# Kernel tuning notes

Hardware: AMD Instinct MI355X
Metric: run time of the kernel (lower is better)

The kernel has to match this reference:

```python
import jax, jax.numpy as jnp
import numpy as np

B, S, D_MODEL = 2, 2048, 4096
N_HEADS, N_KV, HEAD_DIM = 32, 8, 128
N_GROUPS = N_HEADS // N_KV
QKV_DIM = (N_HEADS + 2 * N_KV) * HEAD_DIM


def _rope_tables(seq_len, head_dim, base=10000.0):
    inv_freq = 1.0 / (base ** (np.arange(0, head_dim, 2, dtype=np.float32) / head_dim))
    t = np.arange(seq_len, dtype=np.float32)
    freqs = np.outer(t, inv_freq)                      # [S, D/2]
    emb = np.concatenate([freqs, freqs], axis=-1)      # [S, D]
    return jnp.asarray(np.cos(emb)), jnp.asarray(np.sin(emb))


def setup_inputs() -> dict:
    key = jax.random.key(0)
    k1, k2, k3 = jax.random.split(key, 3)
    cos, sin = _rope_tables(S, HEAD_DIM)
    return {
        "hidden_states": jax.random.normal(k1, (B, S, D_MODEL), dtype=jnp.float32),
        "cos": cos,
        "sin": sin,
        "W_qkv": jax.random.normal(k2, (D_MODEL, QKV_DIM), dtype=jnp.float32) * (D_MODEL ** -0.5),
        "W_out": jax.random.normal(k3, (D_MODEL, D_MODEL), dtype=jnp.float32) * (D_MODEL ** -0.5),
    }


def _rotate_half(x):
    x1, x2 = jnp.split(x, 2, axis=-1)
    return jnp.concatenate([-x2, x1], axis=-1)


def _apply_rope(x, cos, sin):
    # x: [b, h, s, d]; cos/sin: [s, d]
    c = cos[None, None, :, :]
    s = sin[None, None, :, :]
    return x * c + _rotate_half(x) * s


def reference(hidden_states, cos, sin, W_qkv, W_out):
    b, s, _ = hidden_states.shape
    qkv = jnp.einsum("bsm,mq->bsq", hidden_states, W_qkv)
    q_end = N_HEADS * HEAD_DIM
    kv_sz = N_KV * HEAD_DIM
    q = qkv[..., :q_end].reshape(b, s, N_HEADS, HEAD_DIM).transpose(0, 2, 1, 3)
    k = qkv[..., q_end:q_end + kv_sz].reshape(b, s, N_KV, HEAD_DIM).transpose(0, 2, 1, 3)
    v = qkv[..., q_end + kv_sz:].reshape(b, s, N_KV, HEAD_DIM).transpose(0, 2, 1, 3)

    q = _apply_rope(q, cos, sin)          # [b, H, s, d]
    k = _apply_rope(k, cos, sin)          # [b, KV, s, d] (equiv. to repeat->rope->stride slice)

    # GQA without materializing repeated KV: group query heads per KV head.
    qg = q.reshape(b, N_KV, N_GROUPS, s, HEAD_DIM)
    scale = HEAD_DIM ** -0.5
    scores = jnp.einsum("bkgqd,bkpd->bkgqp", qg, k) * scale  # [b, KV, G, s, s]
    causal = jnp.tril(jnp.ones((s, s), dtype=bool))
    scores = jnp.where(causal, scores, jnp.finfo(scores.dtype).min)
    probs = jax.nn.softmax(scores, axis=-1)
    out = jnp.einsum("bkgqp,bkpd->bkgqd", probs, v)           # [b, KV, G, s, d]
    out = out.reshape(b, N_HEADS, s, HEAD_DIM).transpose(0, 2, 1, 3).reshape(b, s, D_MODEL)
    return jnp.einsum("bsm,mn->bsn", out, W_out)
```

## Files before the change

kernel.cpp:

```cpp
#include <hip/hip_runtime.h>


typedef __bf16 bf16;
typedef bf16 bf16x8 __attribute__((ext_vector_type(8)));
typedef bf16 bf16x4 __attribute__((ext_vector_type(4)));
typedef float f32x4 __attribute__((ext_vector_type(4)));
typedef unsigned int u32;
typedef u32 u32x4 __attribute__((ext_vector_type(4)));

#define B_ 2
#define S_ 2048
#define DM 4096
#define NH 32
#define NKV 8
#define HD 128
#define QKV_DIM 6144

typedef __attribute__((address_space(3))) void lds_void;
typedef const __attribute__((address_space(1))) void glb_void;

__device__ __forceinline__ void gld_lds16(const bf16* g, bf16* l) {
  __builtin_amdgcn_global_load_lds((glb_void*)g, (lds_void*)l, 16, 0, 0);
}

__device__ __forceinline__ u32 bf16bits(float x) {
  union { bf16 h; unsigned short s; } u;
  u.h = (bf16)x;
  return (u32)u.s;
}

__global__ __launch_bounds__(256) void cast_f32_bf16(const float* __restrict__ src,
                                                     bf16* __restrict__ dst, int n) {
  int i = (blockIdx.x * 256 + threadIdx.x) * 4;
  float4 v = *(const float4*)(src + i);
  bf16x4 o;
  o[0] = (bf16)v.x; o[1] = (bf16)v.y; o[2] = (bf16)v.z; o[3] = (bf16)v.w;
  *(bf16x4*)(dst + i) = o;
}

__global__ __launch_bounds__(256) void transpose_cast_w(const float* __restrict__ W,
                                                        bf16* __restrict__ Wt,
                                                        int K, int N) {
  __shared__ float tile[64][65];
  const int n0 = blockIdx.x * 64, k0 = blockIdx.y * 64;
  const int t = threadIdx.x, j = t & 63, i0 = t >> 6;
  for (int p = 0; p < 16; ++p) {
    int i = i0 + p * 4;
    tile[i][j] = W[(size_t)(k0 + i) * N + n0 + j];
  }
  __syncthreads();
  for (int p = 0; p < 16; ++p) {
    int n = i0 + p * 4;
    Wt[(size_t)(n0 + n) * K + k0 + j] = (bf16)tile[j][n];
  }
}

__global__ __launch_bounds__(256) void transpose_v(const bf16* __restrict__ qkv,
                                                   bf16* __restrict__ v_t) {
  __shared__ bf16 tile[64][65];
  const int s0 = blockIdx.x * 64;
  const int d0 = blockIdx.y * 64;
  const int bk = blockIdx.z;
  const int b = bk >> 3, kv = bk & 7;
  const int t = threadIdx.x, j = t & 63, i0 = t >> 6;
  const bf16* src = qkv + (size_t)b * S_ * QKV_DIM + 5120 + kv * HD;
  for (int p = 0; p < 16; ++p) {
    int i = i0 + p * 4;
    tile[i][j] = src[(size_t)(s0 + i) * QKV_DIM + d0 + j];
  }
  __syncthreads();
  bf16* dst = v_t + ((size_t)bk * HD + d0) * S_ + s0;
  for (int p = 0; p < 16; ++p) {
    int dd = i0 + p * 4;
    dst[(size_t)dd * S_ + j] = tile[j][dd];
  }
}

__global__ __launch_bounds__(128) void rope_kernel(const bf16* __restrict__ qkv,
                                                   const float* __restrict__ cosT,
                                                   const float* __restrict__ sinT,
                                                   bf16* __restrict__ q_r,
                                                   bf16* __restrict__ k_r) {
  const int bs = blockIdx.x;
  const int b = bs >> 11, s = bs & 2047;
  const int d = threadIdx.x;
  const float cv = cosT[s * HD + d];
  const float sv = sinT[s * HD + d];
  const bf16* row = qkv + (size_t)bs * QKV_DIM;
  const float scale = 0.08838834764831845f;
  for (int h = 0; h < NH; ++h) {
    float x = (float)row[h * HD + d];
    float xr = (d < 64) ? -(float)row[h * HD + d + 64] : (float)row[h * HD + d - 64];
    q_r[(((size_t)(b * NH + h)) * S_ + s) * HD + d] = (bf16)((x * cv + xr * sv) * scale);
  }
  for (int kv = 0; kv < NKV; ++kv) {
    float x = (float)row[DM + kv * HD + d];
    float xr = (d < 64) ? -(float)row[DM + kv * HD + d + 64] : (float)row[DM + kv * HD + d - 64];
    k_r[(((size_t)(b * NKV + kv)) * S_ + s) * HD + d] = (bf16)(x * cv + xr * sv);
  }
}

template <bool OUT_BF16>
__global__ __launch_bounds__(256) void gemm_bt(const bf16* __restrict__ A,
                                               const bf16* __restrict__ Bt,
                                               void* __restrict__ Cout,
                                               int M, int N, int K) {
  __shared__ bf16 As[128 * 32];
  __shared__ bf16 Bs[128 * 32];
  const int m0 = blockIdx.y * 128, n0 = blockIdx.x * 128;
  const int t = threadIdx.x;
  const int lane = t & 63, w = t >> 6;
  const int wm = (w >> 1) * 64, wn = (w & 1) * 64;
  const int quad = lane >> 4, c = lane & 15;

  f32x4 acc[4][4] = {};

  const int s0i = t;
  const int r0 = s0i >> 2, c0 = (s0i & 3) * 8;
  const int s1i = 256 + t;
  const int r1 = s1i >> 2, c1 = (s1i & 3) * 8;
  const bf16* Ap0 = A + (size_t)(m0 + r0) * K + c0;
  const bf16* Ap1 = A + (size_t)(m0 + r1) * K + c1;
  const bf16* Bp0 = Bt + (size_t)(n0 + r0) * K + c0;
  const bf16* Bp1 = Bt + (size_t)(n0 + r1) * K + c1;
  bf16* Asl0 = As + (size_t)(w * 64) * 8;
  bf16* Asl1 = As + (size_t)(256 + w * 64) * 8;
  bf16* Bsl0 = Bs + (size_t)(w * 64) * 8;
  bf16* Bsl1 = Bs + (size_t)(256 + w * 64) * 8;

  for (int k0 = 0; k0 < K; k0 += 32) {
    gld_lds16(Ap0 + k0, Asl0);
    gld_lds16(Ap1 + k0, Asl1);
    gld_lds16(Bp0 + k0, Bsl0);
    gld_lds16(Bp1 + k0, Bsl1);
    __syncthreads();

    bf16x8 af[4], bfr[4];
#pragma unroll
    for (int i = 0; i < 4; ++i)
      af[i] = *(const bf16x8*)(As + (wm + i * 16 + c) * 32 + quad * 8);
#pragma unroll
    for (int j = 0; j < 4; ++j)
      bfr[j] = *(const bf16x8*)(Bs + (wn + j * 16 + c) * 32 + quad * 8);
#pragma unroll
    for (int i = 0; i < 4; ++i)
#pragma unroll
      for (int j = 0; j < 4; ++j)
        acc[i][j] = __builtin_amdgcn_mfma_f32_16x16x32_bf16(af[i], bfr[j], acc[i][j], 0, 0, 0);
    __syncthreads();
  }

#pragma unroll
  for (int i = 0; i < 4; ++i)
#pragma unroll
    for (int j = 0; j < 4; ++j) {
      const int row = m0 + wm + i * 16 + quad * 4;
      const int col = n0 + wn + j * 16 + c;
      if constexpr (OUT_BF16) {
        bf16* Cp = (bf16*)Cout;
#pragma unroll
        for (int r = 0; r < 4; ++r) Cp[(size_t)(row + r) * N + col] = (bf16)acc[i][j][r];
      } else {
        float* Cp = (float*)Cout;
#pragma unroll
        for (int r = 0; r < 4; ++r) Cp[(size_t)(row + r) * N + col] = acc[i][j][r];
      }
    }
}

#define SKS 136
#define SVS 40
__global__ __launch_bounds__(256) void attn_kernel(const bf16* __restrict__ q_r,
                                                   const bf16* __restrict__ k_r,
                                                   const bf16* __restrict__ v_t,
                                                   bf16* __restrict__ attn_out) {
  __shared__ bf16 Ks[32 * SKS];
  __shared__ bf16 Vs[128 * SVS];

  const int bh = blockIdx.x;
  const int b = bh >> 5, h = bh & 31;
  const int kv = h >> 2;
  const int q0 = blockIdx.y * 64;
  const int t = threadIdx.x, w = t >> 6, lane = t & 63;
  const int quad = lane >> 4, c = lane & 15;
  const int myq = q0 + w * 16 + c;

  const bf16* qrow = q_r + ((size_t)(b * NH + h) * S_ + myq) * HD;
  bf16x8 qf[4];
#pragma unroll
  for (int kk = 0; kk < 4; ++kk) qf[kk] = *(const bf16x8*)(qrow + quad * 8 + kk * 32);

  float m_i = -1e30f, l_i = 0.f;
  f32x4 o_acc[8];
#pragma unroll
  for (int n = 0; n < 8; ++n) o_acc[n] = (f32x4){0.f, 0.f, 0.f, 0.f};

  const bf16* kb_ptr = k_r + (size_t)(b * NKV + kv) * S_ * HD;
  const bf16* vb_ptr = v_t + (size_t)(b * NKV + kv) * HD * S_;

  const int nch = (q0 + 64) >> 5;
  const int ks_key = t >> 3, ks_doff = (t & 7) * 16;
  const int vs_d = t >> 1, vs_koff = (t & 1) * 16;
  const int src0 = c + 32 * (quad & 1);
  const int src1 = src0 + 16;
  const bool hiTile = (quad & 2) != 0;

  for (int ch = 0; ch < nch; ++ch) {
    const int kb = ch * 32;
    __syncthreads();
    {
      const bf16* kp = kb_ptr + (size_t)(kb + ks_key) * HD + ks_doff;
      bf16x8 kv0 = *(const bf16x8*)(kp);
      bf16x8 kv1 = *(const bf16x8*)(kp + 8);
      const bf16* vp = vb_ptr + (size_t)vs_d * S_ + kb + vs_koff;
      bf16x8 vv0 = *(const bf16x8*)(vp);
      bf16x8 vv1 = *(const bf16x8*)(vp + 8);
      *(bf16x8*)(Ks + ks_key * SKS + ks_doff) = kv0;
      *(bf16x8*)(Ks + ks_key * SKS + ks_doff + 8) = kv1;
      *(bf16x8*)(Vs + vs_d * SVS + vs_koff) = vv0;
      *(bf16x8*)(Vs + vs_d * SVS + vs_koff + 8) = vv1;
    }
    __syncthreads();

    if (kb <= q0 + w * 16 + 15) {
      f32x4 st0 = (f32x4){0.f, 0.f, 0.f, 0.f};
      f32x4 st1 = (f32x4){0.f, 0.f, 0.f, 0.f};
#pragma unroll
      for (int kk = 0; kk < 4; ++kk) {
        bf16x8 kf0 = *(const bf16x8*)(Ks + c * SKS + quad * 8 + kk * 32);
        bf16x8 kf1 = *(const bf16x8*)(Ks + (16 + c) * SKS + quad * 8 + kk * 32);
        st0 = __builtin_amdgcn_mfma_f32_16x16x32_bf16(kf0, qf[kk], st0, 0, 0, 0);
        st1 = __builtin_amdgcn_mfma_f32_16x16x32_bf16(kf1, qf[kk], st1, 0, 0, 0);
      }

      float v0[4], v1[4];
      const bool needMask = (kb + 31 > q0 + w * 16);
#pragma unroll
      for (int r = 0; r < 4; ++r) { v0[r] = st0[r]; v1[r] = st1[r]; }
      if (needMask) {
        const int key0 = kb + quad * 4;
#pragma unroll
        for (int r = 0; r < 4; ++r) {
          if (key0 + r > myq) v0[r] = -1e30f;
          if (key0 + 16 + r > myq) v1[r] = -1e30f;
        }
      }

      float mloc = fmaxf(fmaxf(fmaxf(v0[0], v0[1]), fmaxf(v0[2], v0[3])),
                         fmaxf(fmaxf(v1[0], v1[1]), fmaxf(v1[2], v1[3])));
      mloc = fmaxf(mloc, __shfl_xor(mloc, 16, 64));
      mloc = fmaxf(mloc, __shfl_xor(mloc, 32, 64));
      const float mnew = fmaxf(m_i, mloc);
      float e0[4], e1[4];
      float sum = 0.f;
#pragma unroll
      for (int r = 0; r < 4; ++r) {
        e0[r] = __expf(v0[r] - mnew);
        e1[r] = __expf(v1[r] - mnew);
        sum += e0[r] + e1[r];
      }
      sum += __shfl_xor(sum, 16, 64);
      sum += __shfl_xor(sum, 32, 64);
      const float alpha = __expf(m_i - mnew);
      m_i = mnew;
      l_i = l_i * alpha + sum;

      u32 pk[4];
#pragma unroll
      for (int r = 0; r < 4; ++r) pk[r] = bf16bits(e0[r]) | (bf16bits(e1[r]) << 16);
      u32 a0[4], a1[4];
#pragma unroll
      for (int r = 0; r < 4; ++r) {
        a0[r] = (u32)__shfl((int)pk[r], src0, 64);
        a1[r] = (u32)__shfl((int)pk[r], src1, 64);
      }
      u32 w0, w1, w2, w3;
      if (hiTile) {
        w0 = (a0[0] >> 16) | (a0[1] & 0xffff0000u);
        w1 = (a0[2] >> 16) | (a0[3] & 0xffff0000u);
        w2 = (a1[0] >> 16) | (a1[1] & 0xffff0000u);
        w3 = (a1[2] >> 16) | (a1[3] & 0xffff0000u);
      } else {
        w0 = (a0[0] & 0xffffu) | (a0[1] << 16);
        w1 = (a0[2] & 0xffffu) | (a0[3] << 16);
        w2 = (a1[0] & 0xffffu) | (a1[1] << 16);
        w3 = (a1[2] & 0xffffu) | (a1[3] << 16);
      }
      bf16x8 pf = __builtin_bit_cast(bf16x8, (u32x4){w0, w1, w2, w3});

      float alpha_o[4];
#pragma unroll
      for (int r = 0; r < 4; ++r) alpha_o[r] = __shfl(alpha, quad * 4 + r, 64);

#pragma unroll
      for (int n = 0; n < 8; ++n) {
#pragma unroll
        for (int r = 0; r < 4; ++r) o_acc[n][r] *= alpha_o[r];
      }
#pragma unroll
      for (int n = 0; n < 8; ++n) {
        bf16x8 vf = *(const bf16x8*)(Vs + (n * 16 + c) * SVS + quad * 8);
        o_acc[n] = __builtin_amdgcn_mfma_f32_16x16x32_bf16(pf, vf, o_acc[n], 0, 0, 0);
      }
    }
  }

  float l_o[4];
#pragma unroll
  for (int r = 0; r < 4; ++r) l_o[r] = __shfl(l_i, quad * 4 + r, 64);
#pragma unroll
  for (int n = 0; n < 8; ++n)
#pragma unroll
    for (int r = 0; r < 4; ++r) {
      const int row = q0 + w * 16 + quad * 4 + r;
      const float ov = o_acc[n][r] / l_o[r];
      attn_out[((size_t)b * S_ + row) * DM + h * HD + n * 16 + c] = (bf16)ov;
    }
}

extern "C" void kernel_launch(void* const* d_in, const int* in_sizes, int n_in,
                              void* d_out, int out_size, void* d_ws, size_t ws_size,
                              hipStream_t stream) {
  const float* hidden = (const float*)d_in[0];
  const float* cosT = (const float*)d_in[1];
  const float* sinT = (const float*)d_in[2];
  const float* Wqkv = (const float*)d_in[3];
  const float* Wout = (const float*)d_in[4];
  float* out = (float*)d_out;
  char* ws = (char*)d_ws;

  bf16* WqkvT = (bf16*)(ws + 0);
  bf16* q_r = (bf16*)(ws + 0);
  bf16* k_r = (bf16*)(ws + 33554432);
  bf16* WoutT = (bf16*)(ws + 50331648);
  bf16* h_bf = (bf16*)(ws + 83886080);
  bf16* attn_out = (bf16*)(ws + 83886080);
  bf16* v_t = (bf16*)(ws + 117440512);
  bf16* qkv = (bf16*)d_out;

  cast_f32_bf16<<<dim3(16384), dim3(256), 0, stream>>>(hidden, h_bf, B_ * S_ * DM);
  transpose_cast_w<<<dim3(QKV_DIM / 64, DM / 64), dim3(256), 0, stream>>>(Wqkv, WqkvT, DM, QKV_DIM);
  transpose_cast_w<<<dim3(DM / 64, DM / 64), dim3(256), 0, stream>>>(Wout, WoutT, DM, DM);
  gemm_bt<true><<<dim3(QKV_DIM / 128, (B_ * S_) / 128), dim3(256), 0, stream>>>(
      h_bf, WqkvT, (void*)qkv, B_ * S_, QKV_DIM, DM);
  rope_kernel<<<dim3(B_ * S_), dim3(128), 0, stream>>>(qkv, cosT, sinT, q_r, k_r);
  transpose_v<<<dim3(S_ / 64, HD / 64, B_ * NKV), dim3(256), 0, stream>>>(qkv, v_t);
  attn_kernel<<<dim3(B_ * NH, S_ / 64), dim3(256), 0, stream>>>(q_r, k_r, v_t, attn_out);
  gemm_bt<false><<<dim3(DM / 128, (B_ * S_) / 128), dim3(256), 0, stream>>>(
      attn_out, WoutT, (void*)out, B_ * S_, DM, DM);
}
```

Baseline: 933.1 us.

## Rewrite GEMMs with large double-buffered swizzled tiles and widen attention KV blocks

Replaces the 128x128 GEMM with a 512-thread templated kernel using large tiles (128x384 for QKV, 256x256 for output). It double-buffers 64-wide K slices in dynamic LDS with XOR swizzling, raw barriers, vmcnt waits, setprio around the MFMA blocks and a grid remap for locality. The attention kernel moves to 64-key chunks, prefetches the next K/V chunk into registers, and skips the rescale of running max and output when the max grows by no more than 8. These changes target memory stalls, LDS bank conflicts and per-iteration overhead, at the cost of much higher register and LDS pressure.

```diff
diff --git a/kernel.cpp b/kernel.cpp
--- a/kernel.cpp
+++ b/kernel.cpp
@@ -28,6 +28,12 @@
   u.h = (bf16)x;
   return (u32)u.s;
 }
+
+#define BAR() __builtin_amdgcn_s_barrier()
+#define VM4() asm volatile("s_waitcnt vmcnt(4)" ::: "memory")
+#define VM0() asm volatile("s_waitcnt vmcnt(0)" ::: "memory")
+#define PRIO1() __builtin_amdgcn_s_setprio(1)
+#define PRIO0() __builtin_amdgcn_s_setprio(0)
 
 __global__ __launch_bounds__(256) void cast_f32_bf16(const float* __restrict__ src,
                                                      bf16* __restrict__ dst, int n) {
@@ -100,81 +106,137 @@
   }
 }
 
-template <bool OUT_BF16>
-__global__ __launch_bounds__(256) void gemm_bt(const bf16* __restrict__ A,
-                                               const bf16* __restrict__ Bt,
-                                               void* __restrict__ Cout,
-                                               int M, int N, int K) {
-  __shared__ bf16 As[128 * 32];
-  __shared__ bf16 Bs[128 * 32];
-  const int m0 = blockIdx.y * 128, n0 = blockIdx.x * 128;
+template <bool OUT_BF16, int BM, int BN>
+__global__ __launch_bounds__(512, 2) void gemm_bt(const bf16* __restrict__ A,
+                                                  const bf16* __restrict__ Bt,
+                                                  void* __restrict__ Cout,
+                                                  int M, int N, int K) {
+  constexpr int MF = BM / 32;
+  constexpr int NF = BN / 64;
+  constexpr int NCA = BM / 128;
+  constexpr int NCB = BN / 128;
+  constexpr int AKH = BM * 64;
+  constexpr int BKH = BN * 64;
+  constexpr int BUF = 2 * (AKH + BKH);
+  extern __shared__ char lds[];
+  const int NT = K >> 6;
+
+  const int nwg = gridDim.x;
+  const int cpx = nwg >> 3;
+  const int wg = (blockIdx.x & 7) * cpx + (blockIdx.x >> 3);
+  const int nbx = N / BN;
+  const int bx = wg % nbx, by = wg / nbx;
+  const int m0 = by * BM, n0 = bx * BN;
+
   const int t = threadIdx.x;
-  const int lane = t & 63, w = t >> 6;
-  const int wm = (w >> 1) * 64, wn = (w & 1) * 64;
+  const int w = t >> 6, lane = t & 63;
+  const int wr = w >> 2, wc = w & 3;
   const int quad = lane >> 4, c = lane & 15;
 
-  f32x4 acc[4][4] = {};
-
-  const int s0i = t;
-  const int r0 = s0i >> 2, c0 = (s0i & 3) * 8;
-  const int s1i = 256 + t;
-  const int r1 = s1i >> 2, c1 = (s1i & 3) * 8;
-  const bf16* Ap0 = A + (size_t)(m0 + r0) * K + c0;
-  const bf16* Ap1 = A + (size_t)(m0 + r1) * K + c1;
-  const bf16* Bp0 = Bt + (size_t)(n0 + r0) * K + c0;
-  const bf16* Bp1 = Bt + (size_t)(n0 + r1) * K + c1;
-  bf16* Asl0 = As + (size_t)(w * 64) * 8;
-  bf16* Asl1 = As + (size_t)(256 + w * 64) * 8;
-  bf16* Bsl0 = Bs + (size_t)(w * 64) * 8;
-  bf16* Bsl1 = Bs + (size_t)(256 + w * 64) * 8;
-
-  for (int k0 = 0; k0 < K; k0 += 32) {
-    gld_lds16(Ap0 + k0, Asl0);
-    gld_lds16(Ap1 + k0, Asl1);
-    gld_lds16(Bp0 + k0, Bsl0);
-    gld_lds16(Bp1 + k0, Bsl1);
-    __syncthreads();
-
-    bf16x8 af[4], bfr[4];
-#pragma unroll
-    for (int i = 0; i < 4; ++i)
-      af[i] = *(const bf16x8*)(As + (wm + i * 16 + c) * 32 + quad * 8);
-#pragma unroll
-    for (int j = 0; j < 4; ++j)
-      bfr[j] = *(const bf16x8*)(Bs + (wn + j * 16 + c) * 32 + quad * 8);
-#pragma unroll
-    for (int i = 0; i < 4; ++i)
-#pragma unroll
-      for (int j = 0; j < 4; ++j)
-        acc[i][j] = __builtin_amdgcn_mfma_f32_16x16x32_bf16(af[i], bfr[j], acc[i][j], 0, 0, 0);
-    __syncthreads();
-  }
-
-#pragma unroll
-  for (int i = 0; i < 4; ++i)
-#pragma unroll
-    for (int j = 0; j < 4; ++j) {
-      const int row = m0 + wm + i * 16 + quad * 4;
-      const int col = n0 + wn + j * 16 + c;
+  const int aOff = (((wr * (BM / 2) + c) * 64 + quad * 16) ^ ((c & 8) << 2));
+  const int bOff = 2 * AKH + ((((wc * (BN / 4) + c) * 64 + quad * 16) ^ ((c & 8) << 2)));
+
+  const int scol = (((lane & 3) ^ ((lane >> 4) & 2)) << 3);
+  const bf16* gA[NCA];
+  const bf16* gB[NCB];
+#pragma unroll
+  for (int cc = 0; cc < NCA; ++cc)
+    gA[cc] = A + (size_t)(m0 + w * (BM / 8) + cc * 16 + (lane >> 2)) * K + scol;
+#pragma unroll
+  for (int cc = 0; cc < NCB; ++cc)
+    gB[cc] = Bt + (size_t)(n0 + w * (BN / 8) + cc * 16 + (lane >> 2)) * K + scol;
+
+  auto stageKh = [&](int P, int kh, int ke) {
+    char* ab = lds + P * BUF + kh * AKH + w * (BM * 8);
+#pragma unroll
+    for (int cc = 0; cc < NCA; ++cc) gld_lds16(gA[cc] + ke, (bf16*)(ab + cc * 1024));
+    char* bb = lds + P * BUF + 2 * AKH + kh * BKH + w * (BN * 8);
+#pragma unroll
+    for (int cc = 0; cc < NCB; ++cc) gld_lds16(gB[cc] + ke, (bf16*)(bb + cc * 1024));
+  };
+
+  bf16x8 a0[MF], b0v[NF], a1[MF], b1v[NF];
+  auto ldFr = [&](int P, int kh, bf16x8* av, bf16x8* bv) {
+    const char* ab = lds + P * BUF + kh * AKH + aOff;
+#pragma unroll
+    for (int i = 0; i < MF; ++i) av[i] = *(const bf16x8*)(ab + i * 1024);
+    const char* bb = lds + P * BUF + kh * BKH + bOff;
+#pragma unroll
+    for (int j = 0; j < NF; ++j) bv[j] = *(const bf16x8*)(bb + j * 1024);
+  };
+
+  f32x4 acc[MF][NF];
+#pragma unroll
+  for (int i = 0; i < MF; ++i)
+#pragma unroll
+    for (int j = 0; j < NF; ++j) acc[i][j] = (f32x4){0.f, 0.f, 0.f, 0.f};
+
+  auto mfmac = [&](bf16x8* av, bf16x8* bv) {
+    PRIO1();
+#pragma unroll
+    for (int i = 0; i < MF; ++i)
+#pragma unroll
+      for (int j = 0; j < NF; ++j)
+        acc[i][j] = __builtin_amdgcn_mfma_f32_16x16x32_bf16(av[i], bv[j], acc[i][j], 0, 0, 0);
+    PRIO0();
+  };
+
+  auto gtile = [&](int P, bool S0, bool S1) {
+    BAR();
+    ldFr(P, 0, a0, b0v);
+    if (S0) stageKh(P ^ 1, 1, 96);
+    mfmac(a0, b0v);
+    ldFr(P, 1, a1, b1v);
+    BAR();
+    if (S1) stageKh(P, 0, 128);
+    mfmac(a1, b1v);
+  };
+
+  auto adv = [&]() {
+#pragma unroll
+    for (int cc = 0; cc < NCA; ++cc) gA[cc] += 64;
+#pragma unroll
+    for (int cc = 0; cc < NCB; ++cc) gB[cc] += 64;
+  };
+
+  stageKh(0, 0, 0); stageKh(0, 1, 32); stageKh(1, 0, 64);
+  VM4();
+
+  for (int tt = 0; tt < NT - 2; tt += 2) {
+    gtile(0, true, true); VM4(); adv();
+    gtile(1, true, true); VM4(); adv();
+  }
+  gtile(0, true, false); VM0();
+  gtile(1, false, false);
+
+  const int crow = m0 + wr * (BM / 2) + quad * 4;
+  const int ccol = n0 + wc * (BN / 4) + c;
+#pragma unroll
+  for (int mf = 0; mf < MF; ++mf)
+#pragma unroll
+    for (int nn = 0; nn < NF; ++nn) {
+      const int row = crow + mf * 16;
+      const int col = ccol + nn * 16;
       if constexpr (OUT_BF16) {
         bf16* Cp = (bf16*)Cout;
 #pragma unroll
-        for (int r = 0; r < 4; ++r) Cp[(size_t)(row + r) * N + col] = (bf16)acc[i][j][r];
+        for (int r = 0; r < 4; ++r) Cp[(size_t)(row + r) * N + col] = (bf16)acc[mf][nn][r];
       } else {
         float* Cp = (float*)Cout;
 #pragma unroll
-        for (int r = 0; r < 4; ++r) Cp[(size_t)(row + r) * N + col] = acc[i][j][r];
-      }
-    }
-}
-
+        for (int r = 0; r < 4; ++r) Cp[(size_t)(row + r) * N + col] = acc[mf][nn][r];
+      }
+    }
+}
+
+#define KVB 64
 #define SKS 136
-#define SVS 40
+#define SVS 72
 __global__ __launch_bounds__(256) void attn_kernel(const bf16* __restrict__ q_r,
                                                    const bf16* __restrict__ k_r,
                                                    const bf16* __restrict__ v_t,
                                                    bf16* __restrict__ attn_out) {
-  __shared__ bf16 Ks[32 * SKS];
+  __shared__ bf16 Ks[KVB * SKS];
   __shared__ bf16 Vs[128 * SVS];
 
   const int bh = blockIdx.x;
@@ -198,109 +260,141 @@
   const bf16* kb_ptr = k_r + (size_t)(b * NKV + kv) * S_ * HD;
   const bf16* vb_ptr = v_t + (size_t)(b * NKV + kv) * HD * S_;
 
-  const int nch = (q0 + 64) >> 5;
-  const int ks_key = t >> 3, ks_doff = (t & 7) * 16;
-  const int vs_d = t >> 1, vs_koff = (t & 1) * 16;
+  const int nch = blockIdx.y + 1;
+
+  const int kkey = t >> 2, kdoff = (t & 3) * 32;
+  const int vd = t >> 1, vkoff = (t & 1) * 32;
+  const bf16* kp = kb_ptr + (size_t)kkey * HD + kdoff;
+  const bf16* vp = vb_ptr + (size_t)vd * S_ + vkoff;
+
   const int src0 = c + 32 * (quad & 1);
   const int src1 = src0 + 16;
   const bool hiTile = (quad & 2) != 0;
 
+  auto packP = [&](const float* ea, const float* eb) -> bf16x8 {
+    u32 pk[4];
+#pragma unroll
+    for (int r = 0; r < 4; ++r) pk[r] = bf16bits(ea[r]) | (bf16bits(eb[r]) << 16);
+    u32 a0[4], a1[4];
+#pragma unroll
+    for (int r = 0; r < 4; ++r) {
+      a0[r] = (u32)__shfl((int)pk[r], src0, 64);
+      a1[r] = (u32)__shfl((int)pk[r], src1, 64);
+    }
+    u32 w0, w1, w2, w3;
+    if (hiTile) {
+      w0 = (a0[0] >> 16) | (a0[1] & 0xffff0000u);
+      w1 = (a0[2] >> 16) | (a0[3] & 0xffff0000u);
+      w2 = (a1[0] >> 16) | (a1[1] & 0xffff0000u);
+      w3 = (a1[2] >> 16) | (a1[3] & 0xffff0000u);
+    } else {
+      w0 = (a0[0] & 0xffffu) | (a0[1] << 16);
+      w1 = (a0[2] & 0xffffu) | (a0[3] << 16);
+      w2 = (a1[0] & 0xffffu) | (a1[1] << 16);
+      w3 = (a1[2] & 0xffffu) | (a1[3] << 16);
+    }
+    return __builtin_bit_cast(bf16x8, (u32x4){w0, w1, w2, w3});
+  };
+
+  bf16x8 krg[4], vrg[4];
+#pragma unroll
+  for (int i = 0; i < 4; ++i) {
+    krg[i] = *(const bf16x8*)(kp + i * 8);
+    vrg[i] = *(const bf16x8*)(vp + i * 8);
+  }
+
   for (int ch = 0; ch < nch; ++ch) {
-    const int kb = ch * 32;
+    const int kb = ch * KVB;
     __syncthreads();
-    {
-      const bf16* kp = kb_ptr + (size_t)(kb + ks_key) * HD + ks_doff;
-      bf16x8 kv0 = *(const bf16x8*)(kp);
-      bf16x8 kv1 = *(const bf16x8*)(kp + 8);
-      const bf16* vp = vb_ptr + (size_t)vs_d * S_ + kb + vs_koff;
-      bf16x8 vv0 = *(const bf16x8*)(vp);
-      bf16x8 vv1 = *(const bf16x8*)(vp + 8);
-      *(bf16x8*)(Ks + ks_key * SKS + ks_doff) = kv0;
-      *(bf16x8*)(Ks + ks_key * SKS + ks_doff + 8) = kv1;
-      *(bf16x8*)(Vs + vs_d * SVS + vs_koff) = vv0;
-      *(bf16x8*)(Vs + vs_d * SVS + vs_koff + 8) = vv1;
+#pragma unroll
+    for (int i = 0; i < 4; ++i) {
+      *(bf16x8*)(Ks + kkey * SKS + kdoff + i * 8) = krg[i];
+      *(bf16x8*)(Vs + vd * SVS + vkoff + i * 8) = vrg[i];
+    }
+    if (ch + 1 < nch) {
+      kp += (size_t)KVB * HD;
+      vp += KVB;
+#pragma unroll
+      for (int i = 0; i < 4; ++i) {
+        krg[i] = *(const bf16x8*)(kp + i * 8);
+        vrg[i] = *(const bf16x8*)(vp + i * 8);
+      }
     }
     __syncthreads();
 
     if (kb <= q0 + w * 16 + 15) {
       f32x4 st0 = (f32x4){0.f, 0.f, 0.f, 0.f};
       f32x4 st1 = (f32x4){0.f, 0.f, 0.f, 0.f};
+      f32x4 st2 = (f32x4){0.f, 0.f, 0.f, 0.f};
+      f32x4 st3 = (f32x4){0.f, 0.f, 0.f, 0.f};
 #pragma unroll
       for (int kk = 0; kk < 4; ++kk) {
-        bf16x8 kf0 = *(const bf16x8*)(Ks + c * SKS + quad * 8 + kk * 32);
+        bf16x8 kf0 = *(const bf16x8*)(Ks + (c) * SKS + quad * 8 + kk * 32);
         bf16x8 kf1 = *(const bf16x8*)(Ks + (16 + c) * SKS + quad * 8 + kk * 32);
+        bf16x8 kf2 = *(const bf16x8*)(Ks + (32 + c) * SKS + quad * 8 + kk * 32);
+        bf16x8 kf3 = *(const bf16x8*)(Ks + (48 + c) * SKS + quad * 8 + kk * 32);
         st0 = __builtin_amdgcn_mfma_f32_16x16x32_bf16(kf0, qf[kk], st0, 0, 0, 0);
         st1 = __builtin_amdgcn_mfma_f32_16x16x32_bf16(kf1, qf[kk], st1, 0, 0, 0);
-      }
-
-      float v0[4], v1[4];
-      const bool needMask = (kb + 31 > q0 + w * 16);
-#pragma unroll
-      for (int r = 0; r < 4; ++r) { v0[r] = st0[r]; v1[r] = st1[r]; }
-      if (needMask) {
+        st2 = __builtin_amdgcn_mfma_f32_16x16x32_bf16(kf2, qf[kk], st2, 0, 0, 0);
+        st3 = __builtin_amdgcn_mfma_f32_16x16x32_bf16(kf3, qf[kk], st3, 0, 0, 0);
+      }
+
+      float e0[4], e1[4], e2[4], e3[4];
+#pragma unroll
+      for (int r = 0; r < 4; ++r) { e0[r] = st0[r]; e1[r] = st1[r]; e2[r] = st2[r]; e3[r] = st3[r]; }
+      if (kb + 63 > q0 + w * 16) {
         const int key0 = kb + quad * 4;
 #pragma unroll
         for (int r = 0; r < 4; ++r) {
-          if (key0 + r > myq) v0[r] = -1e30f;
-          if (key0 + 16 + r > myq) v1[r] = -1e30f;
+          if (key0 + r > myq) e0[r] = -1e30f;
+          if (key0 + 16 + r > myq) e1[r] = -1e30f;
+          if (key0 + 32 + r > myq) e2[r] = -1e30f;
+          if (key0 + 48 + r > myq) e3[r] = -1e30f;
         }
       }
 
-      float mloc = fmaxf(fmaxf(fmaxf(v0[0], v0[1]), fmaxf(v0[2], v0[3])),
-                         fmaxf(fmaxf(v1[0], v1[1]), fmaxf(v1[2], v1[3])));
+      float mloc = fmaxf(fmaxf(fmaxf(e0[0], e0[1]), fmaxf(e0[2], e0[3])),
+                         fmaxf(fmaxf(e1[0], e1[1]), fmaxf(e1[2], e1[3])));
+      mloc = fmaxf(mloc, fmaxf(fmaxf(fmaxf(e2[0], e2[1]), fmaxf(e2[2], e2[3])),
+                               fmaxf(fmaxf(e3[0], e3[1]), fmaxf(e3[2], e3[3]))));
       mloc = fmaxf(mloc, __shfl_xor(mloc, 16, 64));
       mloc = fmaxf(mloc, __shfl_xor(mloc, 32, 64));
-      const float mnew = fmaxf(m_i, mloc);
-      float e0[4], e1[4];
+      const bool defer = (__all(mloc - m_i <= 8.0f) != 0);
+      const float mnew = defer ? m_i : fmaxf(m_i, mloc);
       float sum = 0.f;
 #pragma unroll
       for (int r = 0; r < 4; ++r) {
-        e0[r] = __expf(v0[r] - mnew);
-        e1[r] = __expf(v1[r] - mnew);
-        sum += e0[r] + e1[r];
+        e0[r] = __expf(e0[r] - mnew); sum += e0[r];
+        e1[r] = __expf(e1[r] - mnew); sum += e1[r];
+        e2[r] = __expf(e2[r] - mnew); sum += e2[r];
+        e3[r] = __expf(e3[r] - mnew); sum += e3[r];
       }
       sum += __shfl_xor(sum, 16, 64);
       sum += __shfl_xor(sum, 32, 64);
-      const float alpha = __expf(m_i - mnew);
-      m_i = mnew;
-      l_i = l_i * alpha + sum;
-
-      u32 pk[4];
-#pragma unroll
-      for (int r = 0; r < 4; ++r) pk[r] = bf16bits(e0[r]) | (bf16bits(e1[r]) << 16);
-      u32 a0[4], a1[4];
-#pragma unroll
-      for (int r = 0; r < 4; ++r) {
-        a0[r] = (u32)__shfl((int)pk[r], src0, 64);
-        a1[r] = (u32)__shfl((int)pk[r], src1, 64);
-      }
-      u32 w0, w1, w2, w3;
-      if (hiTile) {
-        w0 = (a0[0] >> 16) | (a0[1] & 0xffff0000u);
-        w1 = (a0[2] >> 16) | (a0[3] & 0xffff0000u);
-        w2 = (a1[0] >> 16) | (a1[1] & 0xffff0000u);
-        w3 = (a1[2] >> 16) | (a1[3] & 0xffff0000u);
+      if (!defer) {
+        const float alpha = __expf(m_i - mnew);
+        m_i = mnew;
+        l_i = l_i * alpha + sum;
+        float alpha_o[4];
+#pragma unroll
+        for (int r = 0; r < 4; ++r) alpha_o[r] = __shfl(alpha, quad * 4 + r, 64);
+#pragma unroll
+        for (int n = 0; n < 8; ++n)
+#pragma unroll
+          for (int r = 0; r < 4; ++r) o_acc[n][r] *= alpha_o[r];
       } else {
-        w0 = (a0[0] & 0xffffu) | (a0[1] << 16);
-        w1 = (a0[2] & 0xffffu) | (a0[3] << 16);
-        w2 = (a1[0] & 0xffffu) | (a1[1] << 16);
-        w3 = (a1[2] & 0xffffu) | (a1[3] << 16);
-      }
-      bf16x8 pf = __builtin_bit_cast(bf16x8, (u32x4){w0, w1, w2, w3});
-
-      float alpha_o[4];
-#pragma unroll
-      for (int r = 0; r < 4; ++r) alpha_o[r] = __shfl(alpha, quad * 4 + r, 64);
+        l_i += sum;
+      }
+
+      bf16x8 pf0 = packP(e0, e1);
+      bf16x8 pf1 = packP(e2, e3);
 
 #pragma unroll
       for (int n = 0; n < 8; ++n) {
-#pragma unroll
-        for (int r = 0; r < 4; ++r) o_acc[n][r] *= alpha_o[r];
-      }
-#pragma unroll
-      for (int n = 0; n < 8; ++n) {
-        bf16x8 vf = *(const bf16x8*)(Vs + (n * 16 + c) * SVS + quad * 8);
-        o_acc[n] = __builtin_amdgcn_mfma_f32_16x16x32_bf16(pf, vf, o_acc[n], 0, 0, 0);
+        bf16x8 vf0 = *(const bf16x8*)(Vs + (n * 16 + c) * SVS + quad * 8);
+        o_acc[n] = __builtin_amdgcn_mfma_f32_16x16x32_bf16(pf0, vf0, o_acc[n], 0, 0, 0);
+        bf16x8 vf1 = *(const bf16x8*)(Vs + (n * 16 + c) * SVS + 32 + quad * 8);
+        o_acc[n] = __builtin_amdgcn_mfma_f32_16x16x32_bf16(pf1, vf1, o_acc[n], 0, 0, 0);
       }
     }
   }
@@ -338,14 +432,23 @@
   bf16* v_t = (bf16*)(ws + 117440512);
   bf16* qkv = (bf16*)d_out;
 
+  static bool attr_set = false;
+  if (!attr_set) {
+    hipFuncSetAttribute(reinterpret_cast<const void*>(&gemm_bt<true, 128, 384>),
+                        hipFuncAttributeMaxDynamicSharedMemorySize, 131072);
+    hipFuncSetAttribute(reinterpret_cast<const void*>(&gemm_bt<false, 256, 256>),
+                        hipFuncAttributeMaxDynamicSharedMemorySize, 131072);
+    attr_set = true;
+  }
+
   cast_f32_bf16<<<dim3(16384), dim3(256), 0, stream>>>(hidden, h_bf, B_ * S_ * DM);
   transpose_cast_w<<<dim3(QKV_DIM / 64, DM / 64), dim3(256), 0, stream>>>(Wqkv, WqkvT, DM, QKV_DIM);
   transpose_cast_w<<<dim3(DM / 64, DM / 64), dim3(256), 0, stream>>>(Wout, WoutT, DM, DM);
-  gemm_bt<true><<<dim3(QKV_DIM / 128, (B_ * S_) / 128), dim3(256), 0, stream>>>(
+  gemm_bt<true, 128, 384><<<dim3((QKV_DIM / 384) * ((B_ * S_) / 128)), dim3(512), 131072, stream>>>(
       h_bf, WqkvT, (void*)qkv, B_ * S_, QKV_DIM, DM);
   rope_kernel<<<dim3(B_ * S_), dim3(128), 0, stream>>>(qkv, cosT, sinT, q_r, k_r);
   transpose_v<<<dim3(S_ / 64, HD / 64, B_ * NKV), dim3(256), 0, stream>>>(qkv, v_t);
   attn_kernel<<<dim3(B_ * NH, S_ / 64), dim3(256), 0, stream>>>(q_r, k_r, v_t, attn_out);
-  gemm_bt<false><<<dim3(DM / 128, (B_ * S_) / 128), dim3(256), 0, stream>>>(
+  gemm_bt<false, 256, 256><<<dim3((DM / 256) * ((B_ * S_) / 256)), dim3(512), 131072, stream>>>(
       attn_out, WoutT, (void*)out, B_ * S_, DM, DM);
 }
```

After: 793.9 us. -14.9%, faster.
